# Kernel optimization log

Measured on AMD Instinct MI355X. Metric: run time of the kernel, lower is better.

The kernel has to match this reference:

```python
import jax, jax.numpy as jnp
import numpy as np

J = 24
ROOT = 0
# SMPL kinematic tree parents
PARENTS = [-1, 0, 0, 0, 1, 2, 3, 4, 5, 6, 7, 8, 9, 9, 9, 12, 13, 14, 16, 17, 18, 19, 20, 21]
RES_SCALE = 0.1


def rodrigues(rvec):
    """Axis-angle (..., 3) -> rotation matrix (..., 3, 3)."""
    theta = jnp.linalg.norm(rvec, axis=-1, keepdims=True)          # (...,1)
    axis = rvec / jnp.maximum(theta, 1e-8)
    x, y, z = axis[..., 0], axis[..., 1], axis[..., 2]
    zero = jnp.zeros_like(x)
    K = jnp.stack([zero, -z, y, z, zero, -x, -y, x, zero], axis=-1)
    K = K.reshape(rvec.shape[:-1] + (3, 3))
    s = jnp.sin(theta)[..., None]
    c = jnp.cos(theta)[..., None]
    I = jnp.eye(3, dtype=rvec.dtype)
    return I + s * K + (1.0 - c) * (K @ K)


def _make_T(R, t):
    """(B,3,3),(B,3) -> (B,4,4) homogeneous transform."""
    B = R.shape[0]
    top = jnp.concatenate([R, t[..., None]], axis=-1)              # (B,3,4)
    bottom = jnp.broadcast_to(jnp.array([0., 0., 0., 1.], R.dtype), (B, 1, 4))
    return jnp.concatenate([top, bottom], axis=-2)


def calculate_kinematic(rest_pose, rvecs, root_locs):
    """rest_pose (J,3), rvecs (B,J,3), root_locs (B,3) -> kp (B,J,3), skts (B,J,4,4).
    Sequential tree-structured chain, unrolled over the 24 joints."""
    R = rodrigues(rvecs)                                           # (B,J,3,3)
    B = rvecs.shape[0]
    l2w = [None] * J
    l2w[ROOT] = _make_T(R[:, ROOT], root_locs)
    for j in range(1, J):
        p = PARENTS[j]
        t_local = jnp.broadcast_to(rest_pose[j] - rest_pose[p], (B, 3))
        l2w[j] = l2w[p] @ _make_T(R[:, j], t_local)
    l2w = jnp.stack(l2w, axis=1)                                   # (B,J,4,4)
    kp = l2w[..., :3, 3]                                           # (B,J,3)
    # skts = inverse(l2w) = [R^T, -R^T t]
    Rt = jnp.swapaxes(l2w[..., :3, :3], -1, -2)
    t_inv = -(Rt @ kp[..., None])                                  # (B,J,3,1)
    top = jnp.concatenate([Rt, t_inv], axis=-1)                    # (B,J,3,4)
    bottom = jnp.broadcast_to(jnp.array([0., 0., 0., 1.], l2w.dtype), (B, J, 1, 4))
    skts = jnp.concatenate([top, bottom], axis=-2)                 # (B,J,4,4)
    return kp, skts


def setup_inputs() -> dict:
    key = jax.random.key(0)
    ks = jax.random.split(key, 12)
    N, NU, E, W = 131072, 16384, 16, 128
    skip = N // NU
    din, dout = J * 3 + E, J * 3 + 3
    bones = jax.random.normal(ks[0], (N, J, 3), jnp.float32) * 0.2
    pelvis_buf = jax.random.normal(ks[1], (NU, 3), jnp.float32)
    kp_idxs = jnp.arange(N, dtype=jnp.int64) // skip
    rest_pose = jax.random.normal(ks[2], (J, 3), jnp.float32) * 0.3
    rest_pose = rest_pose.at[ROOT].set(0.0)
    # kp3d root must match pelvis buffer (original asserts allclose)
    kp3d = jnp.zeros((N, J, 3), jnp.float32).at[:, ROOT].set(pelvis_buf[kp_idxs])
    emb_table = jax.random.normal(ks[3], (NU, E), jnp.float32) * 0.02
    def lin(k, fan_in, fan_out):
        lim = 1.0 / np.sqrt(fan_in)
        k1, k2 = jax.random.split(k)
        return (jax.random.uniform(k1, (fan_in, fan_out), jnp.float32, -lim, lim),
                jax.random.uniform(k2, (fan_out,), jnp.float32, -lim, lim))
    W0, b0 = lin(ks[4], din, W)
    W1, b1 = lin(ks[5], W, W)
    W2, b2 = lin(ks[6], W, W)
    W3, b3 = lin(ks[7], W, dout)
    return dict(bones=bones, kp3d=kp3d, kp_idxs=kp_idxs, emb_table=emb_table,
                pelvis_buf=pelvis_buf, rest_pose=rest_pose,
                W0=W0, b0=b0, W1=W1, b1=b1, W2=W2, b2=b2, W3=W3, b3=b3,
                N_unique=NU)


def reference(bones, kp3d, kp_idxs, emb_table, pelvis_buf, rest_pose,
              W0, b0, W1, b1, W2, b2, W3, b3, N_unique):
    N = bones.shape[0]
    skip = N // N_unique
    rvecs = bones[::skip].reshape(N_unique, J * 3)                 # (Nu, 72)
    kp_u = kp_idxs[::skip]
    embs = emb_table[kp_u]                                         # (Nu, 16)
    pelvis = pelvis_buf[kp_u]                                      # (Nu, 3)
    x = jnp.concatenate([rvecs, embs], axis=-1)
    h = jax.nn.relu(x @ W0 + b0)
    h = jax.nn.relu(h @ W1 + b1)
    h = jax.nn.relu(h @ W2 + b2)
    residual = (h @ W3 + b3) * RES_SCALE                           # (Nu, 75)
    rvecs = (rvecs + residual[:, :J * 3]).reshape(N_unique, J, 3)
    pelvis = pelvis + residual[:, J * 3:]
    kp, skts = calculate_kinematic(rest_pose, rvecs, pelvis)
    # expand unique poses back to full batch ('i s ... -> (i s) ...')
    kp = jnp.repeat(kp, skip, axis=0)                              # (N,J,3)
    skts = jnp.repeat(skts, skip, axis=0)                          # (N,J,4,4)
    rvecs = jnp.repeat(rvecs, skip, axis=0)                        # (N,J,3)
    return kp, skts, rvecs
```

## Files before the change

kernel.cpp:

```cpp
#include <hip/hip_runtime.h>
#include <hip/hip_bf16.h>

typedef unsigned short u16;
using f32x4 = __attribute__((ext_vector_type(4))) float;
using s16x8 = __attribute__((ext_vector_type(8))) short;
using u32x4 = __attribute__((ext_vector_type(4))) unsigned int;

#define JNT 24
#define STRX 104
#define STRH 136

__device__ __forceinline__ u16 f2bf(float f) {
    unsigned int x; __builtin_memcpy(&x, &f, 4);
    unsigned int lsb = (x >> 16) & 1u;
    x += 0x7fffu + lsb;
    return (u16)(x >> 16);
}

__global__ void prep_weights(const float* __restrict__ W0, const float* __restrict__ W1,
                             const float* __restrict__ W2, const float* __restrict__ W3,
                             u16* __restrict__ wst) {
    int i = blockIdx.x * 256 + threadIdx.x;
    if (i < 12288) { int n = i / 96, k = i - n * 96; wst[i] = (k < 88) ? f2bf(W0[k * 128 + n]) : (u16)0; return; }
    i -= 12288;
    if (i < 16384) { int n = i >> 7, k = i & 127; wst[12288 + i] = f2bf(W1[k * 128 + n]); return; }
    i -= 16384;
    if (i < 16384) { int n = i >> 7, k = i & 127; wst[28672 + i] = f2bf(W2[k * 128 + n]); return; }
    i -= 16384;
    if (i < 10240) { int n = i >> 7, k = i & 127; wst[45056 + i] = (n < 75) ? f2bf(W3[k * 75 + n]) : (u16)0; }
}

template<int BASE, int CNT>
__device__ __forceinline__ void mlp_l3(const u16* __restrict__ H, const u16* __restrict__ W3t,
                                       const float* __restrict__ b3, float* __restrict__ res,
                                       int row0, int trow, int lr, int lk, int drow) {
    f32x4 acc[CNT];
#pragma unroll
    for (int t = 0; t < CNT; ++t) {
        int col = (BASE + t) * 16 + lr;
        float bv = (col < 75) ? b3[col] : 0.f;
        acc[t] = (f32x4){bv, bv, bv, bv};
    }
#pragma unroll
    for (int ks = 0; ks < 4; ++ks) {
        s16x8 a = *(const s16x8*)&H[(trow + lr) * STRH + ks * 32 + lk];
#pragma unroll
        for (int t = 0; t < CNT; ++t) {
            s16x8 b = *(const s16x8*)&W3t[((BASE + t) * 16 + lr) * 128 + ks * 32 + lk];
            acc[t] = __builtin_amdgcn_mfma_f32_16x16x32_bf16(a, b, acc[t], 0, 0, 0);
        }
    }
#pragma unroll
    for (int t = 0; t < CNT; ++t) {
        int col = (BASE + t) * 16 + lr;
        if (col < 75) {
#pragma unroll
            for (int q = 0; q < 4; ++q)
                res[(size_t)(row0 + trow + drow + q) * 80 + col] = acc[t][q] * 0.1f;
        }
    }
}

__global__ __launch_bounds__(256)
void mlp_kernel(const float* __restrict__ bones, const float* __restrict__ emb,
                const float* __restrict__ b0, const float* __restrict__ b1,
                const float* __restrict__ b2, const float* __restrict__ b3,
                const u16* __restrict__ wst, float* __restrict__ res, int bstride) {
    __shared__ u16 Xs[32 * STRX];
    __shared__ u16 H1[32 * STRH];
    __shared__ u16 H2[32 * STRH];
    const int tid = threadIdx.x;
    const int row0 = blockIdx.x * 32;

    for (int i = tid; i < 32 * 96; i += 256) {
        int r = i / 96, c = i - r * 96;
        int u = row0 + r;
        float v = 0.f;
        if (c < 72)      v = bones[(size_t)u * bstride + c];
        else if (c < 88) v = emb[(size_t)u * 16 + (c - 72)];
        Xs[r * STRX + c] = f2bf(v);
    }
    __syncthreads();

    const int lane = tid & 63;
    const int wave = tid >> 6;
    const int rt = wave >> 1;
    const int nh = wave & 1;
    const int trow = rt * 16;
    const int lr = lane & 15;
    const int lk = (lane >> 4) * 8;
    const int drow = (lane >> 4) * 4;
    const u16* W0t = wst;
    const u16* W1t = wst + 12288;
    const u16* W2t = wst + 28672;
    const u16* W3t = wst + 45056;

    {
        f32x4 acc[4];
#pragma unroll
        for (int t = 0; t < 4; ++t) { float bv = b0[(nh * 4 + t) * 16 + lr]; acc[t] = (f32x4){bv, bv, bv, bv}; }
#pragma unroll
        for (int ks = 0; ks < 3; ++ks) {
            s16x8 a = *(const s16x8*)&Xs[(trow + lr) * STRX + ks * 32 + lk];
#pragma unroll
            for (int t = 0; t < 4; ++t) {
                s16x8 b = *(const s16x8*)&W0t[((nh * 4 + t) * 16 + lr) * 96 + ks * 32 + lk];
                acc[t] = __builtin_amdgcn_mfma_f32_16x16x32_bf16(a, b, acc[t], 0, 0, 0);
            }
        }
#pragma unroll
        for (int t = 0; t < 4; ++t)
#pragma unroll
            for (int q = 0; q < 4; ++q)
                H1[(trow + drow + q) * STRH + (nh * 4 + t) * 16 + lr] = f2bf(fmaxf(acc[t][q], 0.f));
    }
    __syncthreads();
    {
        f32x4 acc[4];
#pragma unroll
        for (int t = 0; t < 4; ++t) { float bv = b1[(nh * 4 + t) * 16 + lr]; acc[t] = (f32x4){bv, bv, bv, bv}; }
#pragma unroll
        for (int ks = 0; ks < 4; ++ks) {
            s16x8 a = *(const s16x8*)&H1[(trow + lr) * STRH + ks * 32 + lk];
#pragma unroll
            for (int t = 0; t < 4; ++t) {
                s16x8 b = *(const s16x8*)&W1t[((nh * 4 + t) * 16 + lr) * 128 + ks * 32 + lk];
                acc[t] = __builtin_amdgcn_mfma_f32_16x16x32_bf16(a, b, acc[t], 0, 0, 0);
            }
        }
        __syncthreads();
#pragma unroll
        for (int t = 0; t < 4; ++t)
#pragma unroll
            for (int q = 0; q < 4; ++q)
                H2[(trow + drow + q) * STRH + (nh * 4 + t) * 16 + lr] = f2bf(fmaxf(acc[t][q], 0.f));
    }
    __syncthreads();
    {
        f32x4 acc[4];
#pragma unroll
        for (int t = 0; t < 4; ++t) { float bv = b2[(nh * 4 + t) * 16 + lr]; acc[t] = (f32x4){bv, bv, bv, bv}; }
#pragma unroll
        for (int ks = 0; ks < 4; ++ks) {
            s16x8 a = *(const s16x8*)&H2[(trow + lr) * STRH + ks * 32 + lk];
#pragma unroll
            for (int t = 0; t < 4; ++t) {
                s16x8 b = *(const s16x8*)&W2t[((nh * 4 + t) * 16 + lr) * 128 + ks * 32 + lk];
                acc[t] = __builtin_amdgcn_mfma_f32_16x16x32_bf16(a, b, acc[t], 0, 0, 0);
            }
        }
        __syncthreads();
#pragma unroll
        for (int t = 0; t < 4; ++t)
#pragma unroll
            for (int q = 0; q < 4; ++q)
                H1[(trow + drow + q) * STRH + (nh * 4 + t) * 16 + lr] = f2bf(fmaxf(acc[t][q], 0.f));
    }
    __syncthreads();
    if (nh == 0) mlp_l3<0, 3>(H1, W3t, b3, res, row0, trow, lr, lk, drow);
    else         mlp_l3<3, 2>(H1, W3t, b3, res, row0, trow, lr, lk, drow);
}

__device__ const int KPARP[32] = {0,0,0,0,1,2,3,4,5,6,7,8,9,9,9,12,13,14,16,17,18,19,20,21,0,0,0,0,0,0,0,0};
__device__ const int KDEPP[32] = {0,1,1,1,2,2,2,3,3,3,4,4,4,4,4,5,5,5,6,6,7,7,8,8,99,99,99,99,99,99,99,99};

__global__ __launch_bounds__(256)
void kin_kernel(const float* __restrict__ bones, const float* __restrict__ pelvis,
                const float* __restrict__ rest, const float* __restrict__ res,
                float* __restrict__ out, int N, int bstride) {
    __shared__ __align__(16) float so[8][528];
    const int tid = threadIdx.x;
    const int wave = tid >> 6, lane = tid & 63;
    const int half = lane >> 5, j = lane & 31;
    const int sloc = wave * 2 + half;
    const size_t u = (size_t)blockIdx.x * 8 + sloc;

    const int par = KPARP[j], dep = KDEPP[j];
    const int plane = (lane & 32) | par;

    float R[3][3] = {{1.f,0.f,0.f},{0.f,1.f,0.f},{0.f,0.f,1.f}};
    float T[3] = {0.f, 0.f, 0.f};
    float rv0 = 0.f, rv1 = 0.f, rv2 = 0.f;

    if (j < JNT) {
        const float* rs = &res[u * 80];
        const float* bn = &bones[u * (size_t)bstride];
        rv0 = bn[j * 3 + 0] + rs[j * 3 + 0];
        rv1 = bn[j * 3 + 1] + rs[j * 3 + 1];
        rv2 = bn[j * 3 + 2] + rs[j * 3 + 2];
        float th = sqrtf(rv0 * rv0 + rv1 * rv1 + rv2 * rv2);
        float s = sinf(th), c = cosf(th);
        float inv = 1.f / fmaxf(th, 1e-8f);
        float ax = rv0 * inv, ay = rv1 * inv, az = rv2 * inv;
        float K[3][3] = {{0.f, -az, ay}, {az, 0.f, -ax}, {-ay, ax, 0.f}};
        float KK[3][3];
#pragma unroll
        for (int r = 0; r < 3; ++r)
#pragma unroll
            for (int cc = 0; cc < 3; ++cc)
                KK[r][cc] = K[r][0] * K[0][cc] + K[r][1] * K[1][cc] + K[r][2] * K[2][cc];
        float omc = 1.f - c;
#pragma unroll
        for (int r = 0; r < 3; ++r)
#pragma unroll
            for (int cc = 0; cc < 3; ++cc)
                R[r][cc] = ((r == cc) ? 1.f : 0.f) + s * K[r][cc] + omc * KK[r][cc];
        if (j == 0) {
#pragma unroll
            for (int cc = 0; cc < 3; ++cc) T[cc] = pelvis[u * 3 + cc] + rs[72 + cc];
        } else {
#pragma unroll
            for (int cc = 0; cc < 3; ++cc) T[cc] = rest[j * 3 + cc] - rest[par * 3 + cc];
        }
    }

    for (int lev = 1; lev <= 8; ++lev) {
        float p00 = __shfl(R[0][0], plane), p01 = __shfl(R[0][1], plane), p02 = __shfl(R[0][2], plane);
        float p10 = __shfl(R[1][0], plane), p11 = __shfl(R[1][1], plane), p12 = __shfl(R[1][2], plane);
        float p20 = __shfl(R[2][0], plane), p21 = __shfl(R[2][1], plane), p22 = __shfl(R[2][2], plane);
        float q0  = __shfl(T[0],   plane), q1  = __shfl(T[1],   plane), q2  = __shfl(T[2],   plane);
        if (dep == lev) {
            float n00 = p00 * R[0][0] + p01 * R[1][0] + p02 * R[2][0];
            float n01 = p00 * R[0][1] + p01 * R[1][1] + p02 * R[2][1];
            float n02 = p00 * R[0][2] + p01 * R[1][2] + p02 * R[2][2];
            float n10 = p10 * R[0][0] + p11 * R[1][0] + p12 * R[2][0];
            float n11 = p10 * R[0][1] + p11 * R[1][1] + p12 * R[2][1];
            float n12 = p10 * R[0][2] + p11 * R[1][2] + p12 * R[2][2];
            float n20 = p20 * R[0][0] + p21 * R[1][0] + p22 * R[2][0];
            float n21 = p20 * R[0][1] + p21 * R[1][1] + p22 * R[2][1];
            float n22 = p20 * R[0][2] + p21 * R[1][2] + p22 * R[2][2];
            float m0  = p00 * T[0] + p01 * T[1] + p02 * T[2] + q0;
            float m1  = p10 * T[0] + p11 * T[1] + p12 * T[2] + q1;
            float m2  = p20 * T[0] + p21 * T[1] + p22 * T[2] + q2;
            R[0][0] = n00; R[0][1] = n01; R[0][2] = n02;
            R[1][0] = n10; R[1][1] = n11; R[1][2] = n12;
            R[2][0] = n20; R[2][1] = n21; R[2][2] = n22;
            T[0] = m0; T[1] = m1; T[2] = m2;
        }
    }

    if (j < JNT) {
        float* kp = &so[sloc][j * 3];
        kp[0] = T[0]; kp[1] = T[1]; kp[2] = T[2];
        float* sk = &so[sloc][72 + j * 16];
#pragma unroll
        for (int r = 0; r < 3; ++r) {
            sk[r * 4 + 0] = R[0][r];
            sk[r * 4 + 1] = R[1][r];
            sk[r * 4 + 2] = R[2][r];
            sk[r * 4 + 3] = -(R[0][r] * T[0] + R[1][r] * T[1] + R[2][r] * T[2]);
        }
        sk[12] = 0.f; sk[13] = 0.f; sk[14] = 0.f; sk[15] = 1.0f;
        float* rv = &so[sloc][456 + j * 3];
        rv[0] = rv0; rv[1] = rv1; rv[2] = rv2;
    }
    __syncthreads();

    const u32x4* ls = (const u32x4*)so;
    u32x4* o4 = (u32x4*)out;
    const size_t r1 = (size_t)N * 18;
    const size_t r2 = (size_t)N * 114;
    for (int i = tid; i < 8 * 1056; i += 256) {
        int s = i / 1056, w = i - s * 1056;
        size_t uu = (size_t)blockIdx.x * 8 + s;
        const u32x4* src; size_t dst;
        if (w < 144)      { src = ls + s * 132 + (w % 18);              dst = uu * 144 + w; }
        else if (w < 912) { int w2 = w - 144;
                            src = ls + s * 132 + 18 + (w2 % 96);        dst = r1 + uu * 768 + w2; }
        else              { int w3 = w - 912;
                            src = ls + s * 132 + 114 + (w3 % 18);       dst = r2 + uu * 144 + w3; }
        __builtin_nontemporal_store(*src, &o4[dst]);
    }
}

extern "C" void kernel_launch(void* const* d_in, const int* in_sizes, int n_in,
                              void* d_out, int out_size, void* d_ws, size_t ws_size,
                              hipStream_t stream) {
    const float* bones  = (const float*)d_in[0];
    const float* emb    = (const float*)d_in[3];
    const float* pelvis = (const float*)d_in[4];
    const float* rest   = (const float*)d_in[5];
    const float* W0 = (const float*)d_in[6];
    const float* b0 = (const float*)d_in[7];
    const float* W1 = (const float*)d_in[8];
    const float* b1 = (const float*)d_in[9];
    const float* W2 = (const float*)d_in[10];
    const float* b2 = (const float*)d_in[11];
    const float* W3 = (const float*)d_in[12];
    const float* b3 = (const float*)d_in[13];

    const int N    = in_sizes[0] / 72;
    const int NU   = in_sizes[3] / 16;
    const int skip = N / NU;
    const int bstride = skip * 72;

    float* res = (float*)d_ws;
    u16* wst   = (u16*)((char*)d_ws + (size_t)NU * 80 * 4);

    prep_weights<<<216, 256, 0, stream>>>(W0, W1, W2, W3, wst);
    mlp_kernel<<<NU / 32, 256, 0, stream>>>(bones, emb, b0, b1, b2, b3, wst, res, bstride);
    kin_kernel<<<NU / 8, 256, 0, stream>>>(bones, pelvis, rest, res, (float*)d_out, N, bstride);
}
```

Measured before the change: 87.33 us.

## Fuse MLP and kinematic-chain kernels, keeping residuals in shared memory

Merges the MLP kernel and the kinematic kernel into one launch. The residuals stay in LDS instead of making a round trip through global workspace, and each block runs the kinematic chain for its 32 poses in four passes before writing the expanded outputs. It also removes a barrier between layer-2 MMA and the H2 write. In exchange the block uses about 76KB of LDS (launch_bounds 256,2), which lowers occupancy. Writing all 32 poses' outputs serially from one block may also reduce store overlap.

```diff
diff --git a/kernel.cpp b/kernel.cpp
--- a/kernel.cpp
+++ b/kernel.cpp
@@ -32,8 +32,8 @@
 
 template<int BASE, int CNT>
 __device__ __forceinline__ void mlp_l3(const u16* __restrict__ H, const u16* __restrict__ W3t,
-                                       const float* __restrict__ b3, float* __restrict__ res,
-                                       int row0, int trow, int lr, int lk, int drow) {
+                                       const float* __restrict__ b3, float* __restrict__ res_s,
+                                       int trow, int lr, int lk, int drow) {
     f32x4 acc[CNT];
 #pragma unroll
     for (int t = 0; t < CNT; ++t) {
@@ -56,19 +56,28 @@
         if (col < 75) {
 #pragma unroll
             for (int q = 0; q < 4; ++q)
-                res[(size_t)(row0 + trow + drow + q) * 80 + col] = acc[t][q] * 0.1f;
-        }
-    }
-}
-
-__global__ __launch_bounds__(256)
-void mlp_kernel(const float* __restrict__ bones, const float* __restrict__ emb,
-                const float* __restrict__ b0, const float* __restrict__ b1,
-                const float* __restrict__ b2, const float* __restrict__ b3,
-                const u16* __restrict__ wst, float* __restrict__ res, int bstride) {
-    __shared__ u16 Xs[32 * STRX];
-    __shared__ u16 H1[32 * STRH];
-    __shared__ u16 H2[32 * STRH];
+                res_s[(trow + drow + q) * 80 + col] = acc[t][q] * 0.1f;
+        }
+    }
+}
+
+__device__ const int KPARP[32] = {0,0,0,0,1,2,3,4,5,6,7,8,9,9,9,12,13,14,16,17,18,19,20,21,0,0,0,0,0,0,0,0};
+__device__ const int KDEPP[32] = {0,1,1,1,2,2,2,3,3,3,4,4,4,4,4,5,5,5,6,6,7,7,8,8,99,99,99,99,99,99,99,99};
+
+__global__ __launch_bounds__(256, 2)
+void fused_kernel(const float* __restrict__ bones, const float* __restrict__ emb,
+                  const float* __restrict__ pelvis, const float* __restrict__ rest,
+                  const float* __restrict__ b0, const float* __restrict__ b1,
+                  const float* __restrict__ b2, const float* __restrict__ b3,
+                  const u16* __restrict__ wst, float* __restrict__ out,
+                  int N, int bstride) {
+    __shared__ __align__(16) unsigned char smem[77824];
+    float* res_s = (float*)smem;
+    u16* Xs = (u16*)(smem + 10240);
+    u16* H1 = (u16*)(smem + 10240 + 6656);
+    u16* H2 = (u16*)(smem + 10240 + 6656 + 8704);
+    float* so = (float*)(smem + 10240);
+
     const int tid = threadIdx.x;
     const int row0 = blockIdx.x * 32;
 
@@ -128,7 +137,6 @@
                 acc[t] = __builtin_amdgcn_mfma_f32_16x16x32_bf16(a, b, acc[t], 0, 0, 0);
             }
         }
-        __syncthreads();
 #pragma unroll
         for (int t = 0; t < 4; ++t)
 #pragma unroll
@@ -157,102 +165,94 @@
                 H1[(trow + drow + q) * STRH + (nh * 4 + t) * 16 + lr] = f2bf(fmaxf(acc[t][q], 0.f));
     }
     __syncthreads();
-    if (nh == 0) mlp_l3<0, 3>(H1, W3t, b3, res, row0, trow, lr, lk, drow);
-    else         mlp_l3<3, 2>(H1, W3t, b3, res, row0, trow, lr, lk, drow);
-}
-
-__device__ const int KPARP[32] = {0,0,0,0,1,2,3,4,5,6,7,8,9,9,9,12,13,14,16,17,18,19,20,21,0,0,0,0,0,0,0,0};
-__device__ const int KDEPP[32] = {0,1,1,1,2,2,2,3,3,3,4,4,4,4,4,5,5,5,6,6,7,7,8,8,99,99,99,99,99,99,99,99};
-
-__global__ __launch_bounds__(256)
-void kin_kernel(const float* __restrict__ bones, const float* __restrict__ pelvis,
-                const float* __restrict__ rest, const float* __restrict__ res,
-                float* __restrict__ out, int N, int bstride) {
-    __shared__ __align__(16) float so[8][528];
-    const int tid = threadIdx.x;
-    const int wave = tid >> 6, lane = tid & 63;
+    if (nh == 0) mlp_l3<0, 3>(H1, W3t, b3, res_s, trow, lr, lk, drow);
+    else         mlp_l3<3, 2>(H1, W3t, b3, res_s, trow, lr, lk, drow);
+    __syncthreads();
+
     const int half = lane >> 5, j = lane & 31;
-    const int sloc = wave * 2 + half;
-    const size_t u = (size_t)blockIdx.x * 8 + sloc;
-
     const int par = KPARP[j], dep = KDEPP[j];
     const int plane = (lane & 32) | par;
 
-    float R[3][3] = {{1.f,0.f,0.f},{0.f,1.f,0.f},{0.f,0.f,1.f}};
-    float T[3] = {0.f, 0.f, 0.f};
-    float rv0 = 0.f, rv1 = 0.f, rv2 = 0.f;
-
-    if (j < JNT) {
-        const float* rs = &res[u * 80];
-        const float* bn = &bones[u * (size_t)bstride];
-        rv0 = bn[j * 3 + 0] + rs[j * 3 + 0];
-        rv1 = bn[j * 3 + 1] + rs[j * 3 + 1];
-        rv2 = bn[j * 3 + 2] + rs[j * 3 + 2];
-        float th = sqrtf(rv0 * rv0 + rv1 * rv1 + rv2 * rv2);
-        float s = sinf(th), c = cosf(th);
-        float inv = 1.f / fmaxf(th, 1e-8f);
-        float ax = rv0 * inv, ay = rv1 * inv, az = rv2 * inv;
-        float K[3][3] = {{0.f, -az, ay}, {az, 0.f, -ax}, {-ay, ax, 0.f}};
-        float KK[3][3];
-#pragma unroll
-        for (int r = 0; r < 3; ++r)
-#pragma unroll
-            for (int cc = 0; cc < 3; ++cc)
-                KK[r][cc] = K[r][0] * K[0][cc] + K[r][1] * K[1][cc] + K[r][2] * K[2][cc];
-        float omc = 1.f - c;
-#pragma unroll
-        for (int r = 0; r < 3; ++r)
-#pragma unroll
-            for (int cc = 0; cc < 3; ++cc)
-                R[r][cc] = ((r == cc) ? 1.f : 0.f) + s * K[r][cc] + omc * KK[r][cc];
-        if (j == 0) {
-#pragma unroll
-            for (int cc = 0; cc < 3; ++cc) T[cc] = pelvis[u * 3 + cc] + rs[72 + cc];
-        } else {
-#pragma unroll
-            for (int cc = 0; cc < 3; ++cc) T[cc] = rest[j * 3 + cc] - rest[par * 3 + cc];
-        }
-    }
-
-    for (int lev = 1; lev <= 8; ++lev) {
-        float p00 = __shfl(R[0][0], plane), p01 = __shfl(R[0][1], plane), p02 = __shfl(R[0][2], plane);
-        float p10 = __shfl(R[1][0], plane), p11 = __shfl(R[1][1], plane), p12 = __shfl(R[1][2], plane);
-        float p20 = __shfl(R[2][0], plane), p21 = __shfl(R[2][1], plane), p22 = __shfl(R[2][2], plane);
-        float q0  = __shfl(T[0],   plane), q1  = __shfl(T[1],   plane), q2  = __shfl(T[2],   plane);
-        if (dep == lev) {
-            float n00 = p00 * R[0][0] + p01 * R[1][0] + p02 * R[2][0];
-            float n01 = p00 * R[0][1] + p01 * R[1][1] + p02 * R[2][1];
-            float n02 = p00 * R[0][2] + p01 * R[1][2] + p02 * R[2][2];
-            float n10 = p10 * R[0][0] + p11 * R[1][0] + p12 * R[2][0];
-            float n11 = p10 * R[0][1] + p11 * R[1][1] + p12 * R[2][1];
-            float n12 = p10 * R[0][2] + p11 * R[1][2] + p12 * R[2][2];
-            float n20 = p20 * R[0][0] + p21 * R[1][0] + p22 * R[2][0];
-            float n21 = p20 * R[0][1] + p21 * R[1][1] + p22 * R[2][1];
-            float n22 = p20 * R[0][2] + p21 * R[1][2] + p22 * R[2][2];
-            float m0  = p00 * T[0] + p01 * T[1] + p02 * T[2] + q0;
-            float m1  = p10 * T[0] + p11 * T[1] + p12 * T[2] + q1;
-            float m2  = p20 * T[0] + p21 * T[1] + p22 * T[2] + q2;
-            R[0][0] = n00; R[0][1] = n01; R[0][2] = n02;
-            R[1][0] = n10; R[1][1] = n11; R[1][2] = n12;
-            R[2][0] = n20; R[2][1] = n21; R[2][2] = n22;
-            T[0] = m0; T[1] = m1; T[2] = m2;
-        }
-    }
-
-    if (j < JNT) {
-        float* kp = &so[sloc][j * 3];
-        kp[0] = T[0]; kp[1] = T[1]; kp[2] = T[2];
-        float* sk = &so[sloc][72 + j * 16];
-#pragma unroll
-        for (int r = 0; r < 3; ++r) {
-            sk[r * 4 + 0] = R[0][r];
-            sk[r * 4 + 1] = R[1][r];
-            sk[r * 4 + 2] = R[2][r];
-            sk[r * 4 + 3] = -(R[0][r] * T[0] + R[1][r] * T[1] + R[2][r] * T[2]);
-        }
-        sk[12] = 0.f; sk[13] = 0.f; sk[14] = 0.f; sk[15] = 1.0f;
-        float* rv = &so[sloc][456 + j * 3];
-        rv[0] = rv0; rv[1] = rv1; rv[2] = rv2;
+    for (int pass = 0; pass < 4; ++pass) {
+        const int sloc = pass * 8 + wave * 2 + half;
+        const size_t u = (size_t)row0 + sloc;
+
+        float R[3][3] = {{1.f,0.f,0.f},{0.f,1.f,0.f},{0.f,0.f,1.f}};
+        float T[3] = {0.f, 0.f, 0.f};
+        float rv0 = 0.f, rv1 = 0.f, rv2 = 0.f;
+
+        if (j < JNT) {
+            const float* rs = &res_s[sloc * 80];
+            const float* bn = &bones[u * (size_t)bstride];
+            rv0 = bn[j * 3 + 0] + rs[j * 3 + 0];
+            rv1 = bn[j * 3 + 1] + rs[j * 3 + 1];
+            rv2 = bn[j * 3 + 2] + rs[j * 3 + 2];
+            float th = sqrtf(rv0 * rv0 + rv1 * rv1 + rv2 * rv2);
+            float s = sinf(th), c = cosf(th);
+            float inv = 1.f / fmaxf(th, 1e-8f);
+            float ax = rv0 * inv, ay = rv1 * inv, az = rv2 * inv;
+            float K[3][3] = {{0.f, -az, ay}, {az, 0.f, -ax}, {-ay, ax, 0.f}};
+            float KK[3][3];
+#pragma unroll
+            for (int r = 0; r < 3; ++r)
+#pragma unroll
+                for (int cc = 0; cc < 3; ++cc)
+                    KK[r][cc] = K[r][0] * K[0][cc] + K[r][1] * K[1][cc] + K[r][2] * K[2][cc];
+            float omc = 1.f - c;
+#pragma unroll
+            for (int r = 0; r < 3; ++r)
+#pragma unroll
+                for (int cc = 0; cc < 3; ++cc)
+                    R[r][cc] = ((r == cc) ? 1.f : 0.f) + s * K[r][cc] + omc * KK[r][cc];
+            if (j == 0) {
+#pragma unroll
+                for (int cc = 0; cc < 3; ++cc) T[cc] = pelvis[u * 3 + cc] + rs[72 + cc];
+            } else {
+#pragma unroll
+                for (int cc = 0; cc < 3; ++cc) T[cc] = rest[j * 3 + cc] - rest[par * 3 + cc];
+            }
+        }
+
+        for (int lev = 1; lev <= 8; ++lev) {
+            float p00 = __shfl(R[0][0], plane), p01 = __shfl(R[0][1], plane), p02 = __shfl(R[0][2], plane);
+            float p10 = __shfl(R[1][0], plane), p11 = __shfl(R[1][1], plane), p12 = __shfl(R[1][2], plane);
+            float p20 = __shfl(R[2][0], plane), p21 = __shfl(R[2][1], plane), p22 = __shfl(R[2][2], plane);
+            float q0  = __shfl(T[0],   plane), q1  = __shfl(T[1],   plane), q2  = __shfl(T[2],   plane);
+            if (dep == lev) {
+                float n00 = p00 * R[0][0] + p01 * R[1][0] + p02 * R[2][0];
+                float n01 = p00 * R[0][1] + p01 * R[1][1] + p02 * R[2][1];
+                float n02 = p00 * R[0][2] + p01 * R[1][2] + p02 * R[2][2];
+                float n10 = p10 * R[0][0] + p11 * R[1][0] + p12 * R[2][0];
+                float n11 = p10 * R[0][1] + p11 * R[1][1] + p12 * R[2][1];
+                float n12 = p10 * R[0][2] + p11 * R[1][2] + p12 * R[2][2];
+                float n20 = p20 * R[0][0] + p21 * R[1][0] + p22 * R[2][0];
+                float n21 = p20 * R[0][1] + p21 * R[1][1] + p22 * R[2][1];
+                float n22 = p20 * R[0][2] + p21 * R[1][2] + p22 * R[2][2];
+                float m0  = p00 * T[0] + p01 * T[1] + p02 * T[2] + q0;
+                float m1  = p10 * T[0] + p11 * T[1] + p12 * T[2] + q1;
+                float m2  = p20 * T[0] + p21 * T[1] + p22 * T[2] + q2;
+                R[0][0] = n00; R[0][1] = n01; R[0][2] = n02;
+                R[1][0] = n10; R[1][1] = n11; R[1][2] = n12;
+                R[2][0] = n20; R[2][1] = n21; R[2][2] = n22;
+                T[0] = m0; T[1] = m1; T[2] = m2;
+            }
+        }
+
+        if (j < JNT) {
+            float* kp = &so[sloc * 528 + j * 3];
+            kp[0] = T[0]; kp[1] = T[1]; kp[2] = T[2];
+            float* sk = &so[sloc * 528 + 72 + j * 16];
+#pragma unroll
+            for (int r = 0; r < 3; ++r) {
+                sk[r * 4 + 0] = R[0][r];
+                sk[r * 4 + 1] = R[1][r];
+                sk[r * 4 + 2] = R[2][r];
+                sk[r * 4 + 3] = -(R[0][r] * T[0] + R[1][r] * T[1] + R[2][r] * T[2]);
+            }
+            sk[12] = 0.f; sk[13] = 0.f; sk[14] = 0.f; sk[15] = 1.0f;
+            float* rv = &so[sloc * 528 + 456 + j * 3];
+            rv[0] = rv0; rv[1] = rv1; rv[2] = rv2;
+        }
     }
     __syncthreads();
 
@@ -260,9 +260,9 @@
     u32x4* o4 = (u32x4*)out;
     const size_t r1 = (size_t)N * 18;
     const size_t r2 = (size_t)N * 114;
-    for (int i = tid; i < 8 * 1056; i += 256) {
+    for (int i = tid; i < 32 * 1056; i += 256) {
         int s = i / 1056, w = i - s * 1056;
-        size_t uu = (size_t)blockIdx.x * 8 + s;
+        size_t uu = (size_t)row0 + s;
         const u32x4* src; size_t dst;
         if (w < 144)      { src = ls + s * 132 + (w % 18);              dst = uu * 144 + w; }
         else if (w < 912) { int w2 = w - 144;
@@ -294,10 +294,10 @@
     const int skip = N / NU;
     const int bstride = skip * 72;
 
-    float* res = (float*)d_ws;
-    u16* wst   = (u16*)((char*)d_ws + (size_t)NU * 80 * 4);
+    u16* wst = (u16*)d_ws;
 
     prep_weights<<<216, 256, 0, stream>>>(W0, W1, W2, W3, wst);
-    mlp_kernel<<<NU / 32, 256, 0, stream>>>(bones, emb, b0, b1, b2, b3, wst, res, bstride);
-    kin_kernel<<<NU / 8, 256, 0, stream>>>(bones, pelvis, rest, res, (float*)d_out, N, bstride);
-}
+    fused_kernel<<<NU / 32, 256, 0, stream>>>(bones, emb, pelvis, rest,
+                                              b0, b1, b2, b3, wst,
+                                              (float*)d_out, N, bstride);
+}
```

Result: slower. 92.06 us (+5.4%).

## Restructure kinematic output write: 4 poses per block, register-replicated stores

Applied to the files above, without the earlier changes.

The kinematic kernel now handles 4 unique poses per block. Two waves compute the chain, and all threads write the results: each thread loads one 16-byte LDS vector once and stores it 8 times to the replicated output positions, replacing the per-element divide/modulo indexing loop. Skeleton rows are written to LDS as vector stores, and one __syncthreads is removed from the MLP layer-1 path. The stores are no longer nontemporal, and half the waves sit idle during the compute phase. Dropping the barrier may race, since the H2 writes could overlap reads of H1 in other waves, though H1 and H2 are separate buffers.

```diff
diff --git a/kernel.cpp b/kernel.cpp
--- a/kernel.cpp
+++ b/kernel.cpp
@@ -128,7 +128,6 @@
                 acc[t] = __builtin_amdgcn_mfma_f32_16x16x32_bf16(a, b, acc[t], 0, 0, 0);
             }
         }
-        __syncthreads();
 #pragma unroll
         for (int t = 0; t < 4; ++t)
 #pragma unroll
@@ -165,111 +164,128 @@
 __device__ const int KDEPP[32] = {0,1,1,1,2,2,2,3,3,3,4,4,4,4,4,5,5,5,6,6,7,7,8,8,99,99,99,99,99,99,99,99};
 
 __global__ __launch_bounds__(256)
-void kin_kernel(const float* __restrict__ bones, const float* __restrict__ pelvis,
-                const float* __restrict__ rest, const float* __restrict__ res,
-                float* __restrict__ out, int N, int bstride) {
-    __shared__ __align__(16) float so[8][528];
+void kin_write_kernel(const float* __restrict__ bones, const float* __restrict__ pelvis,
+                      const float* __restrict__ rest, const float* __restrict__ res,
+                      float* __restrict__ out, int N, int bstride) {
+    __shared__ __align__(16) float so4[4 * 528];
     const int tid = threadIdx.x;
     const int wave = tid >> 6, lane = tid & 63;
     const int half = lane >> 5, j = lane & 31;
-    const int sloc = wave * 2 + half;
-    const size_t u = (size_t)blockIdx.x * 8 + sloc;
-
     const int par = KPARP[j], dep = KDEPP[j];
     const int plane = (lane & 32) | par;
-
-    float R[3][3] = {{1.f,0.f,0.f},{0.f,1.f,0.f},{0.f,0.f,1.f}};
-    float T[3] = {0.f, 0.f, 0.f};
-    float rv0 = 0.f, rv1 = 0.f, rv2 = 0.f;
-
-    if (j < JNT) {
-        const float* rs = &res[u * 80];
-        const float* bn = &bones[u * (size_t)bstride];
-        rv0 = bn[j * 3 + 0] + rs[j * 3 + 0];
-        rv1 = bn[j * 3 + 1] + rs[j * 3 + 1];
-        rv2 = bn[j * 3 + 2] + rs[j * 3 + 2];
-        float th = sqrtf(rv0 * rv0 + rv1 * rv1 + rv2 * rv2);
-        float s = sinf(th), c = cosf(th);
-        float inv = 1.f / fmaxf(th, 1e-8f);
-        float ax = rv0 * inv, ay = rv1 * inv, az = rv2 * inv;
-        float K[3][3] = {{0.f, -az, ay}, {az, 0.f, -ax}, {-ay, ax, 0.f}};
-        float KK[3][3];
-#pragma unroll
-        for (int r = 0; r < 3; ++r)
-#pragma unroll
-            for (int cc = 0; cc < 3; ++cc)
-                KK[r][cc] = K[r][0] * K[0][cc] + K[r][1] * K[1][cc] + K[r][2] * K[2][cc];
-        float omc = 1.f - c;
-#pragma unroll
-        for (int r = 0; r < 3; ++r)
-#pragma unroll
-            for (int cc = 0; cc < 3; ++cc)
-                R[r][cc] = ((r == cc) ? 1.f : 0.f) + s * K[r][cc] + omc * KK[r][cc];
-        if (j == 0) {
-#pragma unroll
-            for (int cc = 0; cc < 3; ++cc) T[cc] = pelvis[u * 3 + cc] + rs[72 + cc];
-        } else {
-#pragma unroll
-            for (int cc = 0; cc < 3; ++cc) T[cc] = rest[j * 3 + cc] - rest[par * 3 + cc];
-        }
-    }
-
-    for (int lev = 1; lev <= 8; ++lev) {
-        float p00 = __shfl(R[0][0], plane), p01 = __shfl(R[0][1], plane), p02 = __shfl(R[0][2], plane);
-        float p10 = __shfl(R[1][0], plane), p11 = __shfl(R[1][1], plane), p12 = __shfl(R[1][2], plane);
-        float p20 = __shfl(R[2][0], plane), p21 = __shfl(R[2][1], plane), p22 = __shfl(R[2][2], plane);
-        float q0  = __shfl(T[0],   plane), q1  = __shfl(T[1],   plane), q2  = __shfl(T[2],   plane);
-        if (dep == lev) {
-            float n00 = p00 * R[0][0] + p01 * R[1][0] + p02 * R[2][0];
-            float n01 = p00 * R[0][1] + p01 * R[1][1] + p02 * R[2][1];
-            float n02 = p00 * R[0][2] + p01 * R[1][2] + p02 * R[2][2];
-            float n10 = p10 * R[0][0] + p11 * R[1][0] + p12 * R[2][0];
-            float n11 = p10 * R[0][1] + p11 * R[1][1] + p12 * R[2][1];
-            float n12 = p10 * R[0][2] + p11 * R[1][2] + p12 * R[2][2];
-            float n20 = p20 * R[0][0] + p21 * R[1][0] + p22 * R[2][0];
-            float n21 = p20 * R[0][1] + p21 * R[1][1] + p22 * R[2][1];
-            float n22 = p20 * R[0][2] + p21 * R[1][2] + p22 * R[2][2];
-            float m0  = p00 * T[0] + p01 * T[1] + p02 * T[2] + q0;
-            float m1  = p10 * T[0] + p11 * T[1] + p12 * T[2] + q1;
-            float m2  = p20 * T[0] + p21 * T[1] + p22 * T[2] + q2;
-            R[0][0] = n00; R[0][1] = n01; R[0][2] = n02;
-            R[1][0] = n10; R[1][1] = n11; R[1][2] = n12;
-            R[2][0] = n20; R[2][1] = n21; R[2][2] = n22;
-            T[0] = m0; T[1] = m1; T[2] = m2;
-        }
-    }
-
-    if (j < JNT) {
-        float* kp = &so[sloc][j * 3];
-        kp[0] = T[0]; kp[1] = T[1]; kp[2] = T[2];
-        float* sk = &so[sloc][72 + j * 16];
-#pragma unroll
-        for (int r = 0; r < 3; ++r) {
-            sk[r * 4 + 0] = R[0][r];
-            sk[r * 4 + 1] = R[1][r];
-            sk[r * 4 + 2] = R[2][r];
-            sk[r * 4 + 3] = -(R[0][r] * T[0] + R[1][r] * T[1] + R[2][r] * T[2]);
-        }
-        sk[12] = 0.f; sk[13] = 0.f; sk[14] = 0.f; sk[15] = 1.0f;
-        float* rv = &so[sloc][456 + j * 3];
-        rv[0] = rv0; rv[1] = rv1; rv[2] = rv2;
-    }
-    __syncthreads();
-
-    const u32x4* ls = (const u32x4*)so;
+    const int row0 = blockIdx.x * 4;
+
+    if (wave < 2) {
+        const int sloc = wave * 2 + half;
+        const size_t u = (size_t)row0 + sloc;
+
+        float R[3][3] = {{1.f,0.f,0.f},{0.f,1.f,0.f},{0.f,0.f,1.f}};
+        float T[3] = {0.f, 0.f, 0.f};
+        float rv0 = 0.f, rv1 = 0.f, rv2 = 0.f;
+
+        if (j < JNT) {
+            const float* rs = &res[u * 80];
+            const float* bn = &bones[u * (size_t)bstride];
+            rv0 = bn[j * 3 + 0] + rs[j * 3 + 0];
+            rv1 = bn[j * 3 + 1] + rs[j * 3 + 1];
+            rv2 = bn[j * 3 + 2] + rs[j * 3 + 2];
+            float th = sqrtf(rv0 * rv0 + rv1 * rv1 + rv2 * rv2);
+            float s = sinf(th), c = cosf(th);
+            float inv = 1.f / fmaxf(th, 1e-8f);
+            float ax = rv0 * inv, ay = rv1 * inv, az = rv2 * inv;
+            float K[3][3] = {{0.f, -az, ay}, {az, 0.f, -ax}, {-ay, ax, 0.f}};
+            float KK[3][3];
+#pragma unroll
+            for (int r = 0; r < 3; ++r)
+#pragma unroll
+                for (int cc = 0; cc < 3; ++cc)
+                    KK[r][cc] = K[r][0] * K[0][cc] + K[r][1] * K[1][cc] + K[r][2] * K[2][cc];
+            float omc = 1.f - c;
+#pragma unroll
+            for (int r = 0; r < 3; ++r)
+#pragma unroll
+                for (int cc = 0; cc < 3; ++cc)
+                    R[r][cc] = ((r == cc) ? 1.f : 0.f) + s * K[r][cc] + omc * KK[r][cc];
+            if (j == 0) {
+#pragma unroll
+                for (int cc = 0; cc < 3; ++cc) T[cc] = pelvis[u * 3 + cc] + rs[72 + cc];
+            } else {
+#pragma unroll
+                for (int cc = 0; cc < 3; ++cc) T[cc] = rest[j * 3 + cc] - rest[par * 3 + cc];
+            }
+        }
+
+        for (int lev = 1; lev <= 8; ++lev) {
+            float p00 = __shfl(R[0][0], plane), p01 = __shfl(R[0][1], plane), p02 = __shfl(R[0][2], plane);
+            float p10 = __shfl(R[1][0], plane), p11 = __shfl(R[1][1], plane), p12 = __shfl(R[1][2], plane);
+            float p20 = __shfl(R[2][0], plane), p21 = __shfl(R[2][1], plane), p22 = __shfl(R[2][2], plane);
+            float q0  = __shfl(T[0],   plane), q1  = __shfl(T[1],   plane), q2  = __shfl(T[2],   plane);
+            if (dep == lev) {
+                float n00 = p00 * R[0][0] + p01 * R[1][0] + p02 * R[2][0];
+                float n01 = p00 * R[0][1] + p01 * R[1][1] + p02 * R[2][1];
+                float n02 = p00 * R[0][2] + p01 * R[1][2] + p02 * R[2][2];
+                float n10 = p10 * R[0][0] + p11 * R[1][0] + p12 * R[2][0];
+                float n11 = p10 * R[0][1] + p11 * R[1][1] + p12 * R[2][1];
+                float n12 = p10 * R[0][2] + p11 * R[1][2] + p12 * R[2][2];
+                float n20 = p20 * R[0][0] + p21 * R[1][0] + p22 * R[2][0];
+                float n21 = p20 * R[0][1] + p21 * R[1][1] + p22 * R[2][1];
+                float n22 = p20 * R[0][2] + p21 * R[1][2] + p22 * R[2][2];
+                float m0  = p00 * T[0] + p01 * T[1] + p02 * T[2] + q0;
+                float m1  = p10 * T[0] + p11 * T[1] + p12 * T[2] + q1;
+                float m2  = p20 * T[0] + p21 * T[1] + p22 * T[2] + q2;
+                R[0][0] = n00; R[0][1] = n01; R[0][2] = n02;
+                R[1][0] = n10; R[1][1] = n11; R[1][2] = n12;
+                R[2][0] = n20; R[2][1] = n21; R[2][2] = n22;
+                T[0] = m0; T[1] = m1; T[2] = m2;
+            }
+        }
+
+        if (j < JNT) {
+            float* kp = &so4[sloc * 528 + j * 3];
+            kp[0] = T[0]; kp[1] = T[1]; kp[2] = T[2];
+            f32x4* sk4 = (f32x4*)&so4[sloc * 528 + 72 + j * 16];
+#pragma unroll
+            for (int r = 0; r < 3; ++r) {
+                float ti = -(R[0][r] * T[0] + R[1][r] * T[1] + R[2][r] * T[2]);
+                sk4[r] = (f32x4){R[0][r], R[1][r], R[2][r], ti};
+            }
+            sk4[3] = (f32x4){0.f, 0.f, 0.f, 1.f};
+            float* rv = &so4[sloc * 528 + 456 + j * 3];
+            rv[0] = rv0; rv[1] = rv1; rv[2] = rv2;
+        }
+    }
+    __syncthreads();
+
+    const u32x4* ls = (const u32x4*)so4;
     u32x4* o4 = (u32x4*)out;
     const size_t r1 = (size_t)N * 18;
     const size_t r2 = (size_t)N * 114;
-    for (int i = tid; i < 8 * 1056; i += 256) {
-        int s = i / 1056, w = i - s * 1056;
-        size_t uu = (size_t)blockIdx.x * 8 + s;
-        const u32x4* src; size_t dst;
-        if (w < 144)      { src = ls + s * 132 + (w % 18);              dst = uu * 144 + w; }
-        else if (w < 912) { int w2 = w - 144;
-                            src = ls + s * 132 + 18 + (w2 % 96);        dst = r1 + uu * 768 + w2; }
-        else              { int w3 = w - 912;
-                            src = ls + s * 132 + 114 + (w3 % 18);       dst = r2 + uu * 144 + w3; }
-        __builtin_nontemporal_store(*src, &o4[dst]);
+    for (int it = 0; it < 2; ++it) {
+        int idx = tid + it * 256;
+        int s = idx >> 7, p = idx & 127;
+        size_t uu = (size_t)row0 + s;
+        u32x4 v = ls[s * 132 + p];
+        if (p < 18) {
+            u32x4* d = o4 + (uu * 144 + p);
+#pragma unroll
+            for (int rep = 0; rep < 8; ++rep) d[rep * 18] = v;
+        } else if (p < 114) {
+            u32x4* d = o4 + (r1 + uu * 768 + (p - 18));
+#pragma unroll
+            for (int rep = 0; rep < 8; ++rep) d[rep * 96] = v;
+        } else {
+            u32x4* d = o4 + (r2 + uu * 144 + (p - 114));
+#pragma unroll
+            for (int rep = 0; rep < 8; ++rep) d[rep * 18] = v;
+        }
+    }
+    if (tid < 16) {
+        int s = tid >> 2, p = 128 + (tid & 3);
+        size_t uu = (size_t)row0 + s;
+        u32x4 v = ls[s * 132 + p];
+        u32x4* d = o4 + (r2 + uu * 144 + (p - 114));
+#pragma unroll
+        for (int rep = 0; rep < 8; ++rep) d[rep * 18] = v;
     }
 }
 
@@ -299,5 +315,6 @@
 
     prep_weights<<<216, 256, 0, stream>>>(W0, W1, W2, W3, wst);
     mlp_kernel<<<NU / 32, 256, 0, stream>>>(bones, emb, b0, b1, b2, b3, wst, res, bstride);
-    kin_kernel<<<NU / 8, 256, 0, stream>>>(bones, pelvis, rest, res, (float*)d_out, N, bstride);
-}
+    kin_write_kernel<<<NU / 4, 256, 0, stream>>>(bones, pelvis, rest, res,
+                                                 (float*)d_out, N, bstride);
+}
```

Result: faster. 78.35 us (-10.3%).
